# Kernel optimization log

Measured on AMD Instinct MI355X. Metric: run time of the kernel, lower is better.

## Reference

```python
import jax, jax.numpy as jnp
import numpy as np

N_NODES = 4096
HIDDEN = 64
N_REL = 8
N_LAYERS = 2


def setup_inputs() -> dict:
    key = jax.random.key(0)
    k0, k1, k2, k3, k4 = jax.random.split(key, 5)
    node_embed = jax.random.normal(k0, (N_NODES + 1, HIDDEN), dtype=jnp.float32)
    w_self = jax.random.normal(k1, (N_LAYERS, HIDDEN, HIDDEN), dtype=jnp.float32) * 0.02
    w_rel = jax.random.normal(k2, (N_LAYERS, N_REL, HIDDEN, HIDDEN), dtype=jnp.float32) * 0.02
    # dense per-relation adjacency buffer [R, N, N]
    rel_adj = jax.random.uniform(k3, (N_REL, N_NODES, N_NODES), dtype=jnp.float32)
    keyword_ids = jax.random.randint(k4, (64, 32), 0, N_NODES + 1)  # pad id == N_NODES
    return {"node_embed": node_embed, "w_self": w_self, "w_rel": w_rel,
            "rel_adj": rel_adj, "keyword_ids": keyword_ids}


def reference(node_embed, w_self, w_rel, rel_adj, keyword_ids):
    num_nodes = rel_adj.shape[1]
    h = node_embed[:num_nodes]  # [N, D]
    for l in range(w_self.shape[0]):
        out = h @ w_self[l]                                   # self loop [N, D]
        msg = jnp.einsum('rnm,md->rnd', rel_adj, h)           # per-relation aggregation
        out = out + jnp.einsum('rnd,rde->ne', msg, w_rel[l])  # per-relation projection, summed over r
        h = jax.nn.relu(out)
    pad = jnp.zeros((1, h.shape[1]), dtype=h.dtype)
    full_plus_pad = jnp.concatenate([h, pad], axis=0)  # [N+1, D]
    return full_plus_pad[keyword_ids]                  # [B, K, D]
```

## Files before the change

### kernel.cpp

```cpp
#include <hip/hip_runtime.h>

#define N_NODES 4096
#define HID 64
#define NH (N_NODES * HID)

typedef float f32x4 __attribute__((ext_vector_type(4)));
typedef short s16x8 __attribute__((ext_vector_type(8)));

__device__ __forceinline__ short f2bf(float f) {
    union { float f; unsigned u; } v; v.f = f;
    unsigned r = v.u + 0x7fffu + ((v.u >> 16) & 1u);
    return (short)(r >> 16);
}

__global__ __launch_bounds__(256) void proj_kernel(
    const float* __restrict__ h, const float* __restrict__ w_self_l,
    const float* __restrict__ w_rel_l, float* __restrict__ S,
    short* __restrict__ BT)
{
    __shared__ float hs[64][65];
    __shared__ float wt[64][64];
    const int tid = threadIdx.x;
    const int mb = blockIdx.x;
    const int p = blockIdx.y;
    const float* w = (p < 8) ? (w_rel_l + p * 64 * 64) : w_self_l;

    #pragma unroll
    for (int i = 0; i < 4; ++i) {
        int idx4 = tid + 256 * i;
        int row = idx4 >> 4, c = idx4 & 15;
        float4 v = *((const float4*)(h + (size_t)(mb * 64 + row) * HID) + c);
        hs[row][c * 4 + 0] = v.x; hs[row][c * 4 + 1] = v.y;
        hs[row][c * 4 + 2] = v.z; hs[row][c * 4 + 3] = v.w;
    }
    #pragma unroll
    for (int i = 0; i < 4; ++i) {
        int idx4 = tid + 256 * i;
        ((float4*)wt)[idx4] = ((const float4*)w)[idx4];
    }
    __syncthreads();

    const int m = tid & 63;
    const int eb = (tid >> 6) * 16;
    float acc[16];
    #pragma unroll
    for (int j = 0; j < 16; ++j) acc[j] = 0.f;

    #pragma unroll 4
    for (int d = 0; d < 64; ++d) {
        float hv = hs[m][d];
        const float4* wr = (const float4*)&wt[d][eb];
        float4 w0 = wr[0], w1 = wr[1], w2 = wr[2], w3 = wr[3];
        acc[0]  += hv * w0.x; acc[1]  += hv * w0.y; acc[2]  += hv * w0.z; acc[3]  += hv * w0.w;
        acc[4]  += hv * w1.x; acc[5]  += hv * w1.y; acc[6]  += hv * w1.z; acc[7]  += hv * w1.w;
        acc[8]  += hv * w2.x; acc[9]  += hv * w2.y; acc[10] += hv * w2.z; acc[11] += hv * w2.w;
        acc[12] += hv * w3.x; acc[13] += hv * w3.y; acc[14] += hv * w3.z; acc[15] += hv * w3.w;
    }

    if (p < 8) {
        #pragma unroll
        for (int j = 0; j < 16; ++j)
            BT[(size_t)(p * 64 + eb + j) * N_NODES + mb * 64 + m] = f2bf(acc[j]);
    } else {
        #pragma unroll
        for (int j = 0; j < 16; ++j)
            S[(size_t)(mb * 64 + m) * HID + eb + j] = acc[j];
    }
}

__global__ __launch_bounds__(256) void gemm_kernel(
    const float* __restrict__ A, const short* __restrict__ BT,
    float* __restrict__ msg)
{
    const int tid = threadIdx.x;
    const int gid = blockIdx.x;
    const int r  = gid & 7;
    const int rb = (gid >> 3) & 63;
    const int ks = gid >> 9;
    const int wave = tid >> 6, lane = tid & 63;
    const int quad = lane >> 4, l16 = lane & 15;

    const int row = rb * 64 + wave * 16 + l16;
    const float* arow = A + ((size_t)r * N_NODES + row) * N_NODES + ks * 2048 + quad * 8;
    const short* bbase = BT + ((size_t)r * 64 + l16) * N_NODES + ks * 2048 + quad * 8;

    f32x4 acc[4];
    #pragma unroll
    for (int nb = 0; nb < 4; ++nb) acc[nb] = (f32x4){0.f, 0.f, 0.f, 0.f};

    #pragma unroll 2
    for (int k = 0; k < 2048; k += 32) {
        f32x4 a0 = __builtin_nontemporal_load((const f32x4*)(arow + k));
        f32x4 a1 = __builtin_nontemporal_load((const f32x4*)(arow + k + 4));
        s16x8 af;
        af[0] = f2bf(a0[0]); af[1] = f2bf(a0[1]); af[2] = f2bf(a0[2]); af[3] = f2bf(a0[3]);
        af[4] = f2bf(a1[0]); af[5] = f2bf(a1[1]); af[6] = f2bf(a1[2]); af[7] = f2bf(a1[3]);
        #pragma unroll
        for (int nb = 0; nb < 4; ++nb) {
            s16x8 bfr = *(const s16x8*)(bbase + (size_t)nb * 16 * N_NODES + k);
            acc[nb] = __builtin_amdgcn_mfma_f32_16x16x32_bf16(af, bfr, acc[nb], 0, 0, 0);
        }
    }

    float* mo = msg + ((size_t)(r * 2 + ks)) * NH;
    #pragma unroll
    for (int nb = 0; nb < 4; ++nb) {
        #pragma unroll
        for (int i = 0; i < 4; ++i) {
            int orow = rb * 64 + wave * 16 + quad * 4 + i;
            mo[(size_t)orow * HID + nb * 16 + l16] = acc[nb][i];
        }
    }
}

__global__ __launch_bounds__(256) void relu_kernel(
    const float* __restrict__ S, const float* __restrict__ msg, float* __restrict__ hout)
{
    int i = blockIdx.x * 256 + threadIdx.x;
    float4 s = ((const float4*)S)[i];
    #pragma unroll
    for (int p = 0; p < 16; ++p) {
        float4 m = ((const float4*)(msg + (size_t)p * NH))[i];
        s.x += m.x; s.y += m.y; s.z += m.z; s.w += m.w;
    }
    float4 o;
    o.x = fmaxf(s.x, 0.f); o.y = fmaxf(s.y, 0.f);
    o.z = fmaxf(s.z, 0.f); o.w = fmaxf(s.w, 0.f);
    ((float4*)hout)[i] = o;
}

__global__ __launch_bounds__(256) void gather_kernel(
    const float* __restrict__ h2, const int* __restrict__ kw, float* __restrict__ out)
{
    int e = blockIdx.x * 256 + threadIdx.x;
    int ki = e >> 6, d = e & 63;
    int id = kw[ki];
    out[e] = ((unsigned)id < (unsigned)N_NODES) ? h2[(size_t)id * HID + d] : 0.f;
}

extern "C" void kernel_launch(void* const* d_in, const int* in_sizes, int n_in,
                              void* d_out, int out_size, void* d_ws, size_t ws_size,
                              hipStream_t stream) {
    const float* node_embed = (const float*)d_in[0];
    const float* w_self     = (const float*)d_in[1];
    const float* w_rel      = (const float*)d_in[2];
    const float* rel_adj    = (const float*)d_in[3];
    const int*   kw         = (const int*)d_in[4];
    float* out = (float*)d_out;

    float* msg = (float*)d_ws;
    float* S   = msg + 16 * NH;
    float* h1  = S + NH;
    float* h2  = h1 + NH;
    short* BT  = (short*)(h2 + NH);

    const float* hin = node_embed;
    float* houts[2] = {h1, h2};
    for (int l = 0; l < 2; ++l) {
        proj_kernel<<<dim3(64, 9), 256, 0, stream>>>(
            hin, w_self + (size_t)l * 64 * 64, w_rel + (size_t)l * 8 * 64 * 64, S, BT);
        gemm_kernel<<<1024, 256, 0, stream>>>(rel_adj, BT, msg);
        relu_kernel<<<256, 256, 0, stream>>>(S, msg, houts[l]);
        hin = houts[l];
    }
    gather_kernel<<<512, 256, 0, stream>>>(h2, kw, out);
}
```

Baseline: 975.3 us.

## Split GEMM K into four slices and software-prefetch adjacency loads

The adjacency GEMM now splits K into four chunks of 1024 instead of two of 2048, which doubles the grid to 2048 blocks and the partial message buffers to 32. The inner loop also processes 64 K per iteration and register-prefetches the next iteration's fp32 adjacency loads before converting the current ones. The aim is more memory-level parallelism and latency hiding on the bandwidth-bound read of the 512MB adjacency. In exchange, the reduction kernel must read twice as many partial buffers, and the prefetch uses more registers.

```diff
diff --git a/kernel.cpp b/kernel.cpp
--- a/kernel.cpp
+++ b/kernel.cpp
@@ -3,6 +3,7 @@
 #define N_NODES 4096
 #define HID 64
 #define NH (N_NODES * HID)
+#define NPART 32
 
 typedef float f32x4 __attribute__((ext_vector_type(4)));
 typedef short s16x8 __attribute__((ext_vector_type(8)));
@@ -81,28 +82,60 @@
     const int quad = lane >> 4, l16 = lane & 15;
 
     const int row = rb * 64 + wave * 16 + l16;
-    const float* arow = A + ((size_t)r * N_NODES + row) * N_NODES + ks * 2048 + quad * 8;
-    const short* bbase = BT + ((size_t)r * 64 + l16) * N_NODES + ks * 2048 + quad * 8;
+    const float* arow = A + ((size_t)r * N_NODES + row) * N_NODES + ks * 1024 + quad * 8;
+    const short* bbase = BT + ((size_t)r * 64 + l16) * N_NODES + ks * 1024 + quad * 8;
 
     f32x4 acc[4];
     #pragma unroll
     for (int nb = 0; nb < 4; ++nb) acc[nb] = (f32x4){0.f, 0.f, 0.f, 0.f};
 
-    #pragma unroll 2
-    for (int k = 0; k < 2048; k += 32) {
-        f32x4 a0 = __builtin_nontemporal_load((const f32x4*)(arow + k));
-        f32x4 a1 = __builtin_nontemporal_load((const f32x4*)(arow + k + 4));
-        s16x8 af;
-        af[0] = f2bf(a0[0]); af[1] = f2bf(a0[1]); af[2] = f2bf(a0[2]); af[3] = f2bf(a0[3]);
-        af[4] = f2bf(a1[0]); af[5] = f2bf(a1[1]); af[6] = f2bf(a1[2]); af[7] = f2bf(a1[3]);
-        #pragma unroll
-        for (int nb = 0; nb < 4; ++nb) {
-            s16x8 bfr = *(const s16x8*)(bbase + (size_t)nb * 16 * N_NODES + k);
-            acc[nb] = __builtin_amdgcn_mfma_f32_16x16x32_bf16(af, bfr, acc[nb], 0, 0, 0);
-        }
-    }
-
-    float* mo = msg + ((size_t)(r * 2 + ks)) * NH;
+    f32x4 p0 = __builtin_nontemporal_load((const f32x4*)(arow + 0));
+    f32x4 p1 = __builtin_nontemporal_load((const f32x4*)(arow + 4));
+    f32x4 p2 = __builtin_nontemporal_load((const f32x4*)(arow + 32));
+    f32x4 p3 = __builtin_nontemporal_load((const f32x4*)(arow + 36));
+
+    #pragma unroll 3
+    for (int k = 0; k < 960; k += 64) {
+        f32x4 c0 = p0, c1 = p1, c2 = p2, c3 = p3;
+        p0 = __builtin_nontemporal_load((const f32x4*)(arow + k + 64));
+        p1 = __builtin_nontemporal_load((const f32x4*)(arow + k + 68));
+        p2 = __builtin_nontemporal_load((const f32x4*)(arow + k + 96));
+        p3 = __builtin_nontemporal_load((const f32x4*)(arow + k + 100));
+        s16x8 af0, af1;
+        af0[0] = f2bf(c0[0]); af0[1] = f2bf(c0[1]); af0[2] = f2bf(c0[2]); af0[3] = f2bf(c0[3]);
+        af0[4] = f2bf(c1[0]); af0[5] = f2bf(c1[1]); af0[6] = f2bf(c1[2]); af0[7] = f2bf(c1[3]);
+        af1[0] = f2bf(c2[0]); af1[1] = f2bf(c2[1]); af1[2] = f2bf(c2[2]); af1[3] = f2bf(c2[3]);
+        af1[4] = f2bf(c3[0]); af1[5] = f2bf(c3[1]); af1[6] = f2bf(c3[2]); af1[7] = f2bf(c3[3]);
+        #pragma unroll
+        for (int nb = 0; nb < 4; ++nb) {
+            s16x8 b0 = *(const s16x8*)(bbase + (size_t)nb * 16 * N_NODES + k);
+            acc[nb] = __builtin_amdgcn_mfma_f32_16x16x32_bf16(af0, b0, acc[nb], 0, 0, 0);
+        }
+        #pragma unroll
+        for (int nb = 0; nb < 4; ++nb) {
+            s16x8 b1 = *(const s16x8*)(bbase + (size_t)nb * 16 * N_NODES + k + 32);
+            acc[nb] = __builtin_amdgcn_mfma_f32_16x16x32_bf16(af1, b1, acc[nb], 0, 0, 0);
+        }
+    }
+    {
+        s16x8 af0, af1;
+        af0[0] = f2bf(p0[0]); af0[1] = f2bf(p0[1]); af0[2] = f2bf(p0[2]); af0[3] = f2bf(p0[3]);
+        af0[4] = f2bf(p1[0]); af0[5] = f2bf(p1[1]); af0[6] = f2bf(p1[2]); af0[7] = f2bf(p1[3]);
+        af1[0] = f2bf(p2[0]); af1[1] = f2bf(p2[1]); af1[2] = f2bf(p2[2]); af1[3] = f2bf(p2[3]);
+        af1[4] = f2bf(p3[0]); af1[5] = f2bf(p3[1]); af1[6] = f2bf(p3[2]); af1[7] = f2bf(p3[3]);
+        #pragma unroll
+        for (int nb = 0; nb < 4; ++nb) {
+            s16x8 b0 = *(const s16x8*)(bbase + (size_t)nb * 16 * N_NODES + 960);
+            acc[nb] = __builtin_amdgcn_mfma_f32_16x16x32_bf16(af0, b0, acc[nb], 0, 0, 0);
+        }
+        #pragma unroll
+        for (int nb = 0; nb < 4; ++nb) {
+            s16x8 b1 = *(const s16x8*)(bbase + (size_t)nb * 16 * N_NODES + 992);
+            acc[nb] = __builtin_amdgcn_mfma_f32_16x16x32_bf16(af1, b1, acc[nb], 0, 0, 0);
+        }
+    }
+
+    float* mo = msg + (size_t)(r * 4 + ks) * NH;
     #pragma unroll
     for (int nb = 0; nb < 4; ++nb) {
         #pragma unroll
@@ -118,8 +151,8 @@
 {
     int i = blockIdx.x * 256 + threadIdx.x;
     float4 s = ((const float4*)S)[i];
-    #pragma unroll
-    for (int p = 0; p < 16; ++p) {
+    #pragma unroll 8
+    for (int p = 0; p < NPART; ++p) {
         float4 m = ((const float4*)(msg + (size_t)p * NH))[i];
         s.x += m.x; s.y += m.y; s.z += m.z; s.w += m.w;
     }
@@ -149,7 +182,7 @@
     float* out = (float*)d_out;
 
     float* msg = (float*)d_ws;
-    float* S   = msg + 16 * NH;
+    float* S   = msg + (size_t)NPART * NH;
     float* h1  = S + NH;
     float* h2  = h1 + NH;
     short* BT  = (short*)(h2 + NH);
@@ -159,7 +192,7 @@
     for (int l = 0; l < 2; ++l) {
         proj_kernel<<<dim3(64, 9), 256, 0, stream>>>(
             hin, w_self + (size_t)l * 64 * 64, w_rel + (size_t)l * 8 * 64 * 64, S, BT);
-        gemm_kernel<<<1024, 256, 0, stream>>>(rel_adj, BT, msg);
+        gemm_kernel<<<2048, 256, 0, stream>>>(rel_adj, BT, msg);
         relu_kernel<<<256, 256, 0, stream>>>(S, msg, houts[l]);
         hin = houts[l];
     }
```

Result: slower. 1.048 ms (+7.5%).
